# Performance work log

Hardware: AMD Instinct MI355X
Metric: run time of the kernel (lower is better)

## Reference

```python
import jax, jax.numpy as jnp
import numpy as np

N_HEAD, D_MODEL, D_K, D_V = 16, 1024, 64, 64
B, S = 4, 2048


def setup_inputs() -> dict:
    key = jax.random.key(0)
    ks = jax.random.split(key, 11)
    s = 0.02
    return {
        "q": jax.random.normal(ks[0], (B, S, D_MODEL), jnp.float32),
        "k": jax.random.normal(ks[1], (B, S, D_MODEL), jnp.float32),
        "v": jax.random.normal(ks[2], (B, S, D_MODEL), jnp.float32),
        "Wq": jax.random.normal(ks[3], (D_MODEL, N_HEAD * D_K), jnp.float32) * s,
        "bq": jnp.zeros((N_HEAD * D_K,), jnp.float32),
        "Wk": jax.random.normal(ks[4], (D_MODEL, N_HEAD * D_K), jnp.float32) * s,
        "bk": jnp.zeros((N_HEAD * D_K,), jnp.float32),
        "Wv": jax.random.normal(ks[5], (D_MODEL, N_HEAD * D_V), jnp.float32) * s,
        "bv": jnp.zeros((N_HEAD * D_V,), jnp.float32),
        "Wo": jax.random.normal(ks[6], (N_HEAD * D_V, D_MODEL), jnp.float32) * s,
        "bo": jnp.zeros((D_MODEL,), jnp.float32),
    }


def reference(q, k, v, Wq, bq, Wk, bk, Wv, bv, Wo, bo):
    b, s, _ = q.shape
    # project and split heads: [B,S,H,Dk] -> [B,H,S,Dk]
    qh = (q @ Wq + bq).reshape(b, s, N_HEAD, D_K).transpose(0, 2, 1, 3)
    kh = (k @ Wk + bk).reshape(b, s, N_HEAD, D_K).transpose(0, 2, 1, 3)
    vh = (v @ Wv + bv).reshape(b, s, N_HEAD, D_V).transpose(0, 2, 1, 3)
    scale = 1.0 / jnp.sqrt(jnp.float32(D_K))
    scores = jnp.einsum("bhqd,bhkd->bhqk", qh, kh) * scale  # [B,H,S,S]
    atten = jax.nn.softmax(scores, axis=-1)
    out = jnp.einsum("bhqk,bhkd->bhqd", atten, vh)  # [B,H,S,Dv]
    out = out.transpose(0, 2, 1, 3).reshape(b, s, N_HEAD * D_V)
    return out @ Wo + bo
```

## Files before the change

### kernel.cpp

```cpp
#include <hip/hip_runtime.h>

typedef unsigned short u16;
typedef __attribute__((ext_vector_type(4))) float f32x4;
typedef __attribute__((ext_vector_type(16))) float f32x16;
typedef __attribute__((ext_vector_type(8))) short bf16x8;
typedef __attribute__((ext_vector_type(4))) u16 u16x4;
typedef __attribute__((ext_vector_type(8))) u16 u16x8;

#define MFMA16(a, b, c) __builtin_amdgcn_mfma_f32_16x16x32_bf16((a), (b), (c), 0, 0, 0)
#define MFMA32(a, b, c) __builtin_amdgcn_mfma_f32_32x32x16_bf16((a), (b), (c), 0, 0, 0)

__device__ __forceinline__ u16 f2bf(float f) {
  union { float f; unsigned u; } x; x.f = f;
  unsigned r = x.u + 0x7fffu + ((x.u >> 16) & 1u);
  return (u16)(r >> 16);
}

__device__ __forceinline__ unsigned cvtpk(float lo, float hi) {
  unsigned r;
  asm("v_cvt_pk_bf16_f32 %0, %1, %2" : "=v"(r) : "v"(lo), "v"(hi));
  return r;
}

__device__ __forceinline__ void gl_lds16(const void* g, void* l) {
  __builtin_amdgcn_global_load_lds((const __attribute__((address_space(1))) void*)g,
                                   (__attribute__((address_space(3))) void*)l,
                                   16, 0, 0);
}

__global__ __launch_bounds__(256) void cvt3_k(const float* __restrict__ q, const float* __restrict__ k,
                                              const float* __restrict__ v, u16* __restrict__ dst, int n4) {
  const float* src = blockIdx.y == 0 ? q : (blockIdx.y == 1 ? k : v);
  u16* d = dst + (size_t)blockIdx.y * 8192 * 1024;
  int idx = blockIdx.x * blockDim.x + threadIdx.x;
  int stride = gridDim.x * blockDim.x;
  for (int i = idx; i < n4; i += stride) {
    float4 vv = ((const float4*)src)[i];
    u16x4 o;
    o[0] = f2bf(vv.x); o[1] = f2bf(vv.y); o[2] = f2bf(vv.z); o[3] = f2bf(vv.w);
    ((u16x4*)d)[i] = o;
  }
}

__global__ __launch_bounds__(256) void cvtT_k(const float* __restrict__ W0, const float* __restrict__ W1,
                                              const float* __restrict__ W2, const float* __restrict__ W3,
                                              u16* __restrict__ T0, u16* __restrict__ T1,
                                              u16* __restrict__ T2, u16* __restrict__ T3) {
  __shared__ u16 t[64][72];
  const float* W; u16* T;
  switch (blockIdx.z) {
    case 0: W = W0; T = T0; break;
    case 1: W = W1; T = T1; break;
    case 2: W = W2; T = T2; break;
    default: W = W3; T = T3; break;
  }
  const int tid = threadIdx.x;
  const int tr = blockIdx.x, tc = blockIdx.y;
#pragma unroll
  for (int i = 0; i < 4; ++i) {
    int row = i * 16 + (tid >> 4);
    int c4 = tid & 15;
    float4 v = *(const float4*)&W[(size_t)(tr * 64 + row) * 1024 + tc * 64 + c4 * 4];
    t[row][c4 * 4 + 0] = f2bf(v.x);
    t[row][c4 * 4 + 1] = f2bf(v.y);
    t[row][c4 * 4 + 2] = f2bf(v.z);
    t[row][c4 * 4 + 3] = f2bf(v.w);
  }
  __syncthreads();
#pragma unroll
  for (int i = 0; i < 4; ++i) {
    int orow = i * 16 + (tid >> 4);
    int occ = tid & 15;
    u16x4 o;
#pragma unroll
    for (int j = 0; j < 4; ++j) o[j] = t[occ * 4 + j][orow];
    *(u16x4*)&T[(size_t)(tc * 64 + orow) * 1024 + tr * 64 + occ * 4] = o;
  }
}

__global__ __launch_bounds__(256) void gemm_qkv_k(const u16* __restrict__ Xb, const u16* __restrict__ WTb,
                                                  const float* __restrict__ bq, const float* __restrict__ bk,
                                                  const float* __restrict__ bv,
                                                  u16* __restrict__ Qh, u16* __restrict__ Kh,
                                                  u16* __restrict__ Vt, float qscale) {
  __shared__ u16 As[128 * 64];
  __shared__ u16 Bs[128 * 64];
  const int tid = threadIdx.x;
  const int lane = tid & 63;
  const int w = tid >> 6;
  const int which = blockIdx.y >> 3;
  const int m0 = blockIdx.x * 128;
  const int n0 = (blockIdx.y & 7) * 128;
  const u16* X = Xb + (size_t)which * 8192 * 1024;
  const u16* WT = WTb + (size_t)which * 1024 * 1024;
  const float* bias = which == 0 ? bq : (which == 1 ? bk : bv);
  const int wr = (w >> 1) * 64;
  const int wc = (w & 1) * 64;
  const int srow = lane >> 3;
  const int sch = (lane & 7) * 8;
  f32x4 acc[4][4] = {};

  for (int ks = 0; ks < 16; ++ks) {
    const int k0 = ks * 64;
#pragma unroll
    for (int i = 0; i < 4; ++i) {
      int row = i * 32 + w * 8 + srow;
      gl_lds16(X + (size_t)(m0 + row) * 1024 + k0 + sch, &As[(i * 32 + w * 8) * 64]);
      gl_lds16(WT + (size_t)(n0 + row) * 1024 + k0 + sch, &Bs[(i * 32 + w * 8) * 64]);
    }
    __syncthreads();
#pragma unroll
    for (int kk = 0; kk < 2; ++kk) {
      bf16x8 a[4], b[4];
#pragma unroll
      for (int t = 0; t < 4; ++t) {
        a[t] = *(const bf16x8*)&As[(wr + t * 16 + (lane & 15)) * 64 + kk * 32 + (lane >> 4) * 8];
        b[t] = *(const bf16x8*)&Bs[(wc + t * 16 + (lane & 15)) * 64 + kk * 32 + (lane >> 4) * 8];
      }
#pragma unroll
      for (int mi = 0; mi < 4; ++mi)
#pragma unroll
        for (int ni = 0; ni < 4; ++ni)
          acc[mi][ni] = MFMA16(a[mi], b[ni], acc[mi][ni]);
    }
    __syncthreads();
  }

  const int lr = (lane >> 4) * 4;
  const int lc = lane & 15;
  if (which <= 1) {
    u16* ob = which == 0 ? Qh : Kh;
    float scale = which == 0 ? qscale : 1.0f;
#pragma unroll
    for (int mi = 0; mi < 4; ++mi)
#pragma unroll
      for (int ni = 0; ni < 4; ++ni) {
        int n = n0 + wc + ni * 16 + lc;
        float bb = bias[n];
        int h = n >> 6, d = n & 63;
#pragma unroll
        for (int r = 0; r < 4; ++r) {
          int m = m0 + wr + mi * 16 + lr + r;
          int b = m >> 11, s = m & 2047;
          ob[(((size_t)(b * 16 + h) * 2048 + s) << 6) + d] = f2bf((acc[mi][ni][r] + bb) * scale);
        }
      }
  } else {
#pragma unroll
    for (int mi = 0; mi < 4; ++mi)
#pragma unroll
      for (int ni = 0; ni < 4; ++ni) {
        int n = n0 + wc + ni * 16 + lc;
        float bb = bias[n];
        int h = n >> 6, d = n & 63;
        int m = m0 + wr + mi * 16 + lr;
        int b = m >> 11, s = m & 2047;
        u16x4 pk;
#pragma unroll
        for (int r = 0; r < 4; ++r) pk[r] = f2bf(acc[mi][ni][r] + bb);
        *(u16x4*)&Vt[((size_t)(b * 16 + h) * 64 + d) * 2048 + s] = pk;
      }
  }
}

__global__ __launch_bounds__(256) void gemm_o_k(const u16* __restrict__ X, const u16* __restrict__ WT,
                                                const float* __restrict__ bias, float* __restrict__ out) {
  __shared__ u16 As[128 * 64];
  __shared__ u16 Bs[128 * 64];
  const int tid = threadIdx.x;
  const int lane = tid & 63;
  const int w = tid >> 6;
  const int m0 = blockIdx.x * 128;
  const int n0 = blockIdx.y * 128;
  const int wr = (w >> 1) * 64;
  const int wc = (w & 1) * 64;
  const int srow = lane >> 3;
  const int sch = (lane & 7) * 8;
  f32x4 acc[4][4] = {};

  for (int ks = 0; ks < 16; ++ks) {
    const int k0 = ks * 64;
#pragma unroll
    for (int i = 0; i < 4; ++i) {
      int row = i * 32 + w * 8 + srow;
      gl_lds16(X + (size_t)(m0 + row) * 1024 + k0 + sch, &As[(i * 32 + w * 8) * 64]);
      gl_lds16(WT + (size_t)(n0 + row) * 1024 + k0 + sch, &Bs[(i * 32 + w * 8) * 64]);
    }
    __syncthreads();
#pragma unroll
    for (int kk = 0; kk < 2; ++kk) {
      bf16x8 a[4], b[4];
#pragma unroll
      for (int t = 0; t < 4; ++t) {
        a[t] = *(const bf16x8*)&As[(wr + t * 16 + (lane & 15)) * 64 + kk * 32 + (lane >> 4) * 8];
        b[t] = *(const bf16x8*)&Bs[(wc + t * 16 + (lane & 15)) * 64 + kk * 32 + (lane >> 4) * 8];
      }
#pragma unroll
      for (int mi = 0; mi < 4; ++mi)
#pragma unroll
        for (int ni = 0; ni < 4; ++ni)
          acc[mi][ni] = MFMA16(a[mi], b[ni], acc[mi][ni]);
    }
    __syncthreads();
  }

  const int lr = (lane >> 4) * 4;
  const int lc = lane & 15;
#pragma unroll
  for (int mi = 0; mi < 4; ++mi)
#pragma unroll
    for (int ni = 0; ni < 4; ++ni) {
      int n = n0 + wc + ni * 16 + lc;
      float bb = bias[n];
#pragma unroll
      for (int r = 0; r < 4; ++r) {
        int m = m0 + wr + mi * 16 + lr + r;
        out[(size_t)m * 1024 + n] = acc[mi][ni][r] + bb;
      }
    }
}

__global__ __launch_bounds__(512) void attn_k(const u16* __restrict__ Qh, const u16* __restrict__ Kh,
                                              const u16* __restrict__ Vt, u16* __restrict__ AO) {
  __shared__ u16 SMEM[6 * 64 * 64];
  u16* KL = SMEM;
  u16* VL = SMEM + 3 * 64 * 64;
  const int lane = threadIdx.x & 63, w = threadIdx.x >> 6;
  const int hi = lane >> 5, q = lane & 31;

  const int id = blockIdx.x;
  const int bh = ((id >> 3) & 7) * 8 + (id & 7);
  const int qt = id >> 6;
  const int q0 = qt * 256 + w * 32;

  const u16* Qb = Qh + (size_t)bh * 2048 * 64;
  const u16* Kb = Kh + (size_t)bh * 2048 * 64;
  const u16* Vb = Vt + (size_t)bh * 64 * 2048;

  bf16x8 qf[4];
#pragma unroll
  for (int c = 0; c < 4; ++c)
    qf[c] = *(const bf16x8*)&Qb[(size_t)(q0 + q) * 64 + c * 16 + hi * 8];

  f32x16 o0 = {}, o1 = {};
  float l_ = 0.f;

  const int sr = lane >> 3;
  const int sc8 = ((lane & 7) ^ sr) * 8;

#define STAGE(buf_, kt_) do {                                                     \
    int k0_ = (kt_) * 64;                                                         \
    gl_lds16(Kb + (size_t)(k0_ + w * 8 + sr) * 64 + sc8, &KL[((buf_) * 64 + w * 8) * 64]); \
    gl_lds16(Vb + (size_t)(w * 8 + sr) * 2048 + k0_ + sc8, &VL[((buf_) * 64 + w * 8) * 64]); \
  } while (0)

  STAGE(0, 0);
  STAGE(1, 1);
  STAGE(2, 2);

  for (int kt = 0; kt < 32; ++kt) {
    if (kt < 30) asm volatile("s_waitcnt vmcnt(4)" ::: "memory");
    else         asm volatile("s_waitcnt vmcnt(0)" ::: "memory");
    __builtin_amdgcn_s_barrier();
    __builtin_amdgcn_sched_barrier(0);

    const u16* Kc = &KL[(kt % 3) * 64 * 64];
    const u16* Vc = &VL[(kt % 3) * 64 * 64];

    f32x16 s0 = {}, s1 = {};
    __builtin_amdgcn_s_setprio(1);
#pragma unroll
    for (int c = 0; c < 4; ++c) {
      int ch = c * 2 + hi;
      bf16x8 k0 = *(const bf16x8*)&Kc[q * 64 + ((ch ^ (q & 7)) * 8)];
      bf16x8 k1 = *(const bf16x8*)&Kc[(32 + q) * 64 + ((ch ^ (q & 7)) * 8)];
      s0 = MFMA32(k0, qf[c], s0);
      s1 = MFMA32(k1, qf[c], s1);
    }
    __builtin_amdgcn_s_setprio(0);

#pragma unroll
    for (int i = 0; i < 16; ++i) {
      s0[i] = __builtin_exp2f(s0[i]);
      s1[i] = __builtin_exp2f(s1[i]);
    }
    float sum = 0.f;
#pragma unroll
    for (int i = 0; i < 16; ++i) sum += s0[i] + s1[i];
    l_ += sum;

    __builtin_amdgcn_s_setprio(1);
#pragma unroll
    for (int t = 0; t < 4; ++t) {
      unsigned wA, wB, wC, wD;
      if (t == 0) { wA = cvtpk(s0[0], s0[1]); wB = cvtpk(s0[2], s0[3]); wC = cvtpk(s0[4], s0[5]); wD = cvtpk(s0[6], s0[7]); }
      else if (t == 1) { wA = cvtpk(s0[8], s0[9]); wB = cvtpk(s0[10], s0[11]); wC = cvtpk(s0[12], s0[13]); wD = cvtpk(s0[14], s0[15]); }
      else if (t == 2) { wA = cvtpk(s1[0], s1[1]); wB = cvtpk(s1[2], s1[3]); wC = cvtpk(s1[4], s1[5]); wD = cvtpk(s1[6], s1[7]); }
      else { wA = cvtpk(s1[8], s1[9]); wB = cvtpk(s1[10], s1[11]); wC = cvtpk(s1[12], s1[13]); wD = cvtpk(s1[14], s1[15]); }
      asm("v_permlane32_swap_b32 %0, %1" : "+v"(wA), "+v"(wC));
      asm("v_permlane32_swap_b32 %0, %1" : "+v"(wB), "+v"(wD));
      union { unsigned u[4]; bf16x8 v; } pf;
      pf.u[0] = wA; pf.u[1] = wB; pf.u[2] = wC; pf.u[3] = wD;
      int ch = t * 2 + hi;
      bf16x8 v0 = *(const bf16x8*)&Vc[q * 64 + ((ch ^ (q & 7)) * 8)];
      bf16x8 v1 = *(const bf16x8*)&Vc[(32 + q) * 64 + ((ch ^ (q & 7)) * 8)];
      o0 = MFMA32(v0, pf.v, o0);
      o1 = MFMA32(v1, pf.v, o1);
    }
    __builtin_amdgcn_s_setprio(0);

    __builtin_amdgcn_sched_barrier(0);
    __builtin_amdgcn_s_barrier();
    if (kt < 29) STAGE(kt % 3, kt + 3);
  }
#undef STAGE

  l_ += __shfl_xor(l_, 32);
  u16* ep = SMEM + w * 2048;
  float inv = 1.0f / l_;
#pragma unroll
  for (int g = 0; g < 2; ++g) {
    const f32x16 oo = g ? o1 : o0;
#pragma unroll
    for (int j = 0; j < 8; ++j) {
      int d = g * 32 + (j & 1) * 2 + ((j >> 1) & 1) * 8 + (j >> 2) * 16 + 4 * hi;
      unsigned pw = cvtpk(oo[2 * j] * inv, oo[2 * j + 1] * inv);
      *(unsigned*)&ep[q * 64 + ((d >> 3) ^ (q & 7)) * 8 + (d & 7)] = pw;
    }
  }
  asm volatile("s_waitcnt lgkmcnt(0)" ::: "memory");
  const int b = bh >> 4, h = bh & 15;
#pragma unroll
  for (int i = 0; i < 4; ++i) {
    int r = i * 8 + (lane >> 3), c = lane & 7;
    u16x8 vv = *(const u16x8*)&ep[r * 64 + ((c ^ (r & 7)) * 8)];
    size_t row = (size_t)b * 2048 + q0 + r;
    *(u16x8*)&AO[row * 1024 + h * 64 + c * 8] = vv;
  }
}

extern "C" void kernel_launch(void* const* d_in, const int* in_sizes, int n_in,
                              void* d_out, int out_size, void* d_ws, size_t ws_size,
                              hipStream_t stream) {
  const float* q  = (const float*)d_in[0];
  const float* k  = (const float*)d_in[1];
  const float* v  = (const float*)d_in[2];
  const float* Wq = (const float*)d_in[3];
  const float* bq = (const float*)d_in[4];
  const float* Wk = (const float*)d_in[5];
  const float* bk = (const float*)d_in[6];
  const float* Wv = (const float*)d_in[7];
  const float* bv = (const float*)d_in[8];
  const float* Wo = (const float*)d_in[9];
  const float* bo = (const float*)d_in[10];
  float* out = (float*)d_out;

  char* ws = (char*)d_ws;
  const size_t SZX = (size_t)8192 * 1024 * 2;
  const size_t SZW = (size_t)1024 * 1024 * 2;
  u16* Xq  = (u16*)(ws);
  u16* WTq = (u16*)(ws + 3 * SZX);
  u16* WTk = (u16*)(ws + 3 * SZX + SZW);
  u16* WTv = (u16*)(ws + 3 * SZX + 2 * SZW);
  u16* WTo = (u16*)(ws + 3 * SZX + 3 * SZW);
  u16* Qh  = (u16*)(ws + 3 * SZX + 4 * SZW);
  u16* Kh  = (u16*)(ws + 4 * SZX + 4 * SZW);
  u16* Vt  = (u16*)(ws + 5 * SZX + 4 * SZW);
  u16* AO  = Xq;

  const int n4 = 8192 * 1024 / 4;
  cvt3_k<<<dim3(1024, 3), dim3(256), 0, stream>>>(q, k, v, Xq, n4);
  cvtT_k<<<dim3(16, 16, 4), dim3(256), 0, stream>>>(Wq, Wk, Wv, Wo, WTq, WTk, WTv, WTo);

  gemm_qkv_k<<<dim3(64, 24), dim3(256), 0, stream>>>(Xq, WTq, bq, bk, bv, Qh, Kh, Vt,
                                                     0.125f * 1.4426950408889634f);

  attn_k<<<dim3(512), dim3(512), 0, stream>>>(Qh, Kh, Vt, AO);

  gemm_o_k<<<dim3(64, 8), dim3(256), 0, stream>>>(AO, WTo, bo, out);
}
```

Before: 231.9 us.

## Process 64 query rows per wave in attention to reuse K/V fragments

Halves the attention block to 4 waves and has each wave handle two 32-row query tiles, so every K and V LDS fragment feeds two MFMAs instead of one. Staging issues twice the loads per wave and the vmcnt thresholds are adjusted to match. This targets LDS read traffic per MFMA, at the cost of roughly doubling accumulator and score registers per wave and having fewer waves per block to hide latency.

```diff
diff --git a/kernel.cpp b/kernel.cpp
--- a/kernel.cpp
+++ b/kernel.cpp
@@ -220,7 +220,7 @@
     }
 }
 
-__global__ __launch_bounds__(512) void attn_k(const u16* __restrict__ Qh, const u16* __restrict__ Kh,
+__global__ __launch_bounds__(256) void attn_k(const u16* __restrict__ Qh, const u16* __restrict__ Kh,
                                               const u16* __restrict__ Vt, u16* __restrict__ AO) {
   __shared__ u16 SMEM[6 * 64 * 64];
   u16* KL = SMEM;
@@ -231,27 +231,31 @@
   const int id = blockIdx.x;
   const int bh = ((id >> 3) & 7) * 8 + (id & 7);
   const int qt = id >> 6;
-  const int q0 = qt * 256 + w * 32;
+  const int q0 = qt * 256 + w * 64;
 
   const u16* Qb = Qh + (size_t)bh * 2048 * 64;
   const u16* Kb = Kh + (size_t)bh * 2048 * 64;
   const u16* Vb = Vt + (size_t)bh * 64 * 2048;
 
-  bf16x8 qf[4];
-#pragma unroll
-  for (int c = 0; c < 4; ++c)
-    qf[c] = *(const bf16x8*)&Qb[(size_t)(q0 + q) * 64 + c * 16 + hi * 8];
-
-  f32x16 o0 = {}, o1 = {};
-  float l_ = 0.f;
+  bf16x8 qf0[4], qf1[4];
+#pragma unroll
+  for (int c = 0; c < 4; ++c) {
+    qf0[c] = *(const bf16x8*)&Qb[(size_t)(q0 + q) * 64 + c * 16 + hi * 8];
+    qf1[c] = *(const bf16x8*)&Qb[(size_t)(q0 + 32 + q) * 64 + c * 16 + hi * 8];
+  }
+
+  f32x16 o00 = {}, o01 = {}, o10 = {}, o11 = {};
+  float l0 = 0.f, l1 = 0.f;
 
   const int sr = lane >> 3;
   const int sc8 = ((lane & 7) ^ sr) * 8;
 
-#define STAGE(buf_, kt_) do {                                                     \
-    int k0_ = (kt_) * 64;                                                         \
-    gl_lds16(Kb + (size_t)(k0_ + w * 8 + sr) * 64 + sc8, &KL[((buf_) * 64 + w * 8) * 64]); \
-    gl_lds16(Vb + (size_t)(w * 8 + sr) * 2048 + k0_ + sc8, &VL[((buf_) * 64 + w * 8) * 64]); \
+#define STAGE(buf_, kt_) do {                                                               \
+    int k0_ = (kt_) * 64;                                                                   \
+    gl_lds16(Kb + (size_t)(k0_ + w * 16 + sr) * 64 + sc8,      &KL[((buf_) * 64 + w * 16) * 64]);     \
+    gl_lds16(Kb + (size_t)(k0_ + w * 16 + 8 + sr) * 64 + sc8,  &KL[((buf_) * 64 + w * 16 + 8) * 64]); \
+    gl_lds16(Vb + (size_t)(w * 16 + sr) * 2048 + k0_ + sc8,    &VL[((buf_) * 64 + w * 16) * 64]);     \
+    gl_lds16(Vb + (size_t)(w * 16 + 8 + sr) * 2048 + k0_ + sc8,&VL[((buf_) * 64 + w * 16 + 8) * 64]); \
   } while (0)
 
   STAGE(0, 0);
@@ -259,53 +263,73 @@
   STAGE(2, 2);
 
   for (int kt = 0; kt < 32; ++kt) {
-    if (kt < 30) asm volatile("s_waitcnt vmcnt(4)" ::: "memory");
-    else         asm volatile("s_waitcnt vmcnt(0)" ::: "memory");
+    if (kt < 30)      asm volatile("s_waitcnt vmcnt(8)" ::: "memory");
+    else if (kt == 30) asm volatile("s_waitcnt vmcnt(4)" ::: "memory");
+    else              asm volatile("s_waitcnt vmcnt(0)" ::: "memory");
     __builtin_amdgcn_s_barrier();
     __builtin_amdgcn_sched_barrier(0);
 
     const u16* Kc = &KL[(kt % 3) * 64 * 64];
     const u16* Vc = &VL[(kt % 3) * 64 * 64];
 
-    f32x16 s0 = {}, s1 = {};
+    f32x16 s00 = {}, s01 = {}, s10 = {}, s11 = {};
     __builtin_amdgcn_s_setprio(1);
 #pragma unroll
     for (int c = 0; c < 4; ++c) {
       int ch = c * 2 + hi;
       bf16x8 k0 = *(const bf16x8*)&Kc[q * 64 + ((ch ^ (q & 7)) * 8)];
       bf16x8 k1 = *(const bf16x8*)&Kc[(32 + q) * 64 + ((ch ^ (q & 7)) * 8)];
-      s0 = MFMA32(k0, qf[c], s0);
-      s1 = MFMA32(k1, qf[c], s1);
+      s00 = MFMA32(k0, qf0[c], s00);
+      s01 = MFMA32(k0, qf1[c], s01);
+      s10 = MFMA32(k1, qf0[c], s10);
+      s11 = MFMA32(k1, qf1[c], s11);
     }
     __builtin_amdgcn_s_setprio(0);
 
+    float sum0 = 0.f, sum1 = 0.f;
 #pragma unroll
     for (int i = 0; i < 16; ++i) {
-      s0[i] = __builtin_exp2f(s0[i]);
-      s1[i] = __builtin_exp2f(s1[i]);
-    }
-    float sum = 0.f;
-#pragma unroll
-    for (int i = 0; i < 16; ++i) sum += s0[i] + s1[i];
-    l_ += sum;
+      s00[i] = __builtin_exp2f(s00[i]);
+      s10[i] = __builtin_exp2f(s10[i]);
+      sum0 += s00[i] + s10[i];
+      s01[i] = __builtin_exp2f(s01[i]);
+      s11[i] = __builtin_exp2f(s11[i]);
+      sum1 += s01[i] + s11[i];
+    }
+    l0 += sum0;
+    l1 += sum1;
 
     __builtin_amdgcn_s_setprio(1);
 #pragma unroll
     for (int t = 0; t < 4; ++t) {
-      unsigned wA, wB, wC, wD;
-      if (t == 0) { wA = cvtpk(s0[0], s0[1]); wB = cvtpk(s0[2], s0[3]); wC = cvtpk(s0[4], s0[5]); wD = cvtpk(s0[6], s0[7]); }
-      else if (t == 1) { wA = cvtpk(s0[8], s0[9]); wB = cvtpk(s0[10], s0[11]); wC = cvtpk(s0[12], s0[13]); wD = cvtpk(s0[14], s0[15]); }
-      else if (t == 2) { wA = cvtpk(s1[0], s1[1]); wB = cvtpk(s1[2], s1[3]); wC = cvtpk(s1[4], s1[5]); wD = cvtpk(s1[6], s1[7]); }
-      else { wA = cvtpk(s1[8], s1[9]); wB = cvtpk(s1[10], s1[11]); wC = cvtpk(s1[12], s1[13]); wD = cvtpk(s1[14], s1[15]); }
-      asm("v_permlane32_swap_b32 %0, %1" : "+v"(wA), "+v"(wC));
-      asm("v_permlane32_swap_b32 %0, %1" : "+v"(wB), "+v"(wD));
-      union { unsigned u[4]; bf16x8 v; } pf;
-      pf.u[0] = wA; pf.u[1] = wB; pf.u[2] = wC; pf.u[3] = wD;
+      unsigned a0, a1, a2, a3, b0, b1, b2, b3;
+      if (t == 0) {
+        a0 = cvtpk(s00[0], s00[1]); a1 = cvtpk(s00[2], s00[3]); a2 = cvtpk(s00[4], s00[5]); a3 = cvtpk(s00[6], s00[7]);
+        b0 = cvtpk(s01[0], s01[1]); b1 = cvtpk(s01[2], s01[3]); b2 = cvtpk(s01[4], s01[5]); b3 = cvtpk(s01[6], s01[7]);
+      } else if (t == 1) {
+        a0 = cvtpk(s00[8], s00[9]); a1 = cvtpk(s00[10], s00[11]); a2 = cvtpk(s00[12], s00[13]); a3 = cvtpk(s00[14], s00[15]);
+        b0 = cvtpk(s01[8], s01[9]); b1 = cvtpk(s01[10], s01[11]); b2 = cvtpk(s01[12], s01[13]); b3 = cvtpk(s01[14], s01[15]);
+      } else if (t == 2) {
+        a0 = cvtpk(s10[0], s10[1]); a1 = cvtpk(s10[2], s10[3]); a2 = cvtpk(s10[4], s10[5]); a3 = cvtpk(s10[6], s10[7]);
+        b0 = cvtpk(s11[0], s11[1]); b1 = cvtpk(s11[2], s11[3]); b2 = cvtpk(s11[4], s11[5]); b3 = cvtpk(s11[6], s11[7]);
+      } else {
+        a0 = cvtpk(s10[8], s10[9]); a1 = cvtpk(s10[10], s10[11]); a2 = cvtpk(s10[12], s10[13]); a3 = cvtpk(s10[14], s10[15]);
+        b0 = cvtpk(s11[8], s11[9]); b1 = cvtpk(s11[10], s11[11]); b2 = cvtpk(s11[12], s11[13]); b3 = cvtpk(s11[14], s11[15]);
+      }
+      asm("v_permlane32_swap_b32 %0, %1" : "+v"(a0), "+v"(a2));
+      asm("v_permlane32_swap_b32 %0, %1" : "+v"(a1), "+v"(a3));
+      asm("v_permlane32_swap_b32 %0, %1" : "+v"(b0), "+v"(b2));
+      asm("v_permlane32_swap_b32 %0, %1" : "+v"(b1), "+v"(b3));
+      union { unsigned u[4]; bf16x8 v; } pf0, pf1;
+      pf0.u[0] = a0; pf0.u[1] = a1; pf0.u[2] = a2; pf0.u[3] = a3;
+      pf1.u[0] = b0; pf1.u[1] = b1; pf1.u[2] = b2; pf1.u[3] = b3;
       int ch = t * 2 + hi;
       bf16x8 v0 = *(const bf16x8*)&Vc[q * 64 + ((ch ^ (q & 7)) * 8)];
       bf16x8 v1 = *(const bf16x8*)&Vc[(32 + q) * 64 + ((ch ^ (q & 7)) * 8)];
-      o0 = MFMA32(v0, pf.v, o0);
-      o1 = MFMA32(v1, pf.v, o1);
+      o00 = MFMA32(v0, pf0.v, o00);
+      o01 = MFMA32(v0, pf1.v, o01);
+      o10 = MFMA32(v1, pf0.v, o10);
+      o11 = MFMA32(v1, pf1.v, o11);
     }
     __builtin_amdgcn_s_setprio(0);
 
@@ -315,27 +339,37 @@
   }
 #undef STAGE
 
-  l_ += __shfl_xor(l_, 32);
-  u16* ep = SMEM + w * 2048;
-  float inv = 1.0f / l_;
-#pragma unroll
-  for (int g = 0; g < 2; ++g) {
-    const f32x16 oo = g ? o1 : o0;
-#pragma unroll
-    for (int j = 0; j < 8; ++j) {
-      int d = g * 32 + (j & 1) * 2 + ((j >> 1) & 1) * 8 + (j >> 2) * 16 + 4 * hi;
-      unsigned pw = cvtpk(oo[2 * j] * inv, oo[2 * j + 1] * inv);
-      *(unsigned*)&ep[q * 64 + ((d >> 3) ^ (q & 7)) * 8 + (d & 7)] = pw;
+  l0 += __shfl_xor(l0, 32);
+  l1 += __shfl_xor(l1, 32);
+  const int b = bh >> 4, h = bh & 15;
+  u16* ep = SMEM + w * 4096;
+  float inv0 = 1.0f / l0, inv1 = 1.0f / l1;
+#pragma unroll
+  for (int qh = 0; qh < 2; ++qh) {
+    u16* eph = ep + qh * 2048;
+    float inv = qh ? inv1 : inv0;
+#pragma unroll
+    for (int g = 0; g < 2; ++g) {
+      const f32x16 oo = qh ? (g ? o11 : o01) : (g ? o10 : o00);
+#pragma unroll
+      for (int j = 0; j < 8; ++j) {
+        int d = g * 32 + (j & 1) * 2 + ((j >> 1) & 1) * 8 + (j >> 2) * 16 + 4 * hi;
+        unsigned pw = cvtpk(oo[2 * j] * inv, oo[2 * j + 1] * inv);
+        *(unsigned*)&eph[q * 64 + ((d >> 3) ^ (q & 7)) * 8 + (d & 7)] = pw;
+      }
     }
   }
   asm volatile("s_waitcnt lgkmcnt(0)" ::: "memory");
-  const int b = bh >> 4, h = bh & 15;
-#pragma unroll
-  for (int i = 0; i < 4; ++i) {
-    int r = i * 8 + (lane >> 3), c = lane & 7;
-    u16x8 vv = *(const u16x8*)&ep[r * 64 + ((c ^ (r & 7)) * 8)];
-    size_t row = (size_t)b * 2048 + q0 + r;
-    *(u16x8*)&AO[row * 1024 + h * 64 + c * 8] = vv;
+#pragma unroll
+  for (int qh = 0; qh < 2; ++qh) {
+    u16* eph = ep + qh * 2048;
+#pragma unroll
+    for (int i = 0; i < 4; ++i) {
+      int r = i * 8 + (lane >> 3), c = lane & 7;
+      u16x8 vv = *(const u16x8*)&eph[r * 64 + ((c ^ (r & 7)) * 8)];
+      size_t row = (size_t)b * 2048 + q0 + qh * 32 + r;
+      *(u16x8*)&AO[row * 1024 + h * 64 + c * 8] = vv;
+    }
   }
 }
 
@@ -375,7 +409,7 @@
   gemm_qkv_k<<<dim3(64, 24), dim3(256), 0, stream>>>(Xq, WTq, bq, bk, bv, Qh, Kh, Vt,
                                                      0.125f * 1.4426950408889634f);
 
-  attn_k<<<dim3(512), dim3(512), 0, stream>>>(Qh, Kh, Vt, AO);
+  attn_k<<<dim3(512), dim3(256), 0, stream>>>(Qh, Kh, Vt, AO);
 
   gemm_o_k<<<dim3(64, 8), dim3(256), 0, stream>>>(AO, WTo, bo, out);
 }
```

New measurement: 276.1 us. 19.1% more time.
